# Kernel optimization log

Measured on AMD Instinct MI355X. Metric: run time of the kernel, lower is better.

Reference implementation:

```python
import jax, jax.numpy as jnp
import numpy as np

DIM = 1024
NUM_HEADS = 16
HEAD_DIM = DIM // NUM_HEADS


def setup_inputs() -> dict:
    key = jax.random.key(0)
    k1, k2, k3 = jax.random.split(key, 3)
    x = jax.random.normal(k1, (2, 2048, DIM), dtype=jnp.float32)
    # nn.Linear weights stored as [out, in]; apply as x @ W.T
    w_qkv = jax.random.normal(k2, (3 * DIM, DIM), dtype=jnp.float32) * (1.0 / np.sqrt(DIM))
    w_out = jax.random.normal(k3, (DIM, DIM), dtype=jnp.float32) * (1.0 / np.sqrt(DIM))
    return {"x": x, "w_qkv": w_qkv, "w_out": w_out}


def reference(x, w_qkv, w_out):
    b, t, _ = x.shape
    qkv = x @ w_qkv.T                                  # [b, t, 3*dim]
    qkv = qkv.reshape(b, t, 3, NUM_HEADS, HEAD_DIM)    # (three h d) split order
    q, k, v = jnp.moveaxis(qkv, 2, 0)                  # each [b, t, h, d]
    q = q.transpose(0, 2, 1, 3)                        # [b, h, t, d]
    k = k.transpose(0, 2, 1, 3)
    v = v.transpose(0, 2, 1, 3)
    attn = jnp.einsum('bhid,bhjd->bhij', q, k) / np.sqrt(HEAD_DIM)
    causal_mask = jnp.triu(jnp.ones((t, t), dtype=bool), k=1)
    attn = jnp.where(causal_mask, -jnp.inf, attn)
    attn = jax.nn.softmax(attn, axis=-1)
    out = jnp.einsum('bhij,bhjd->bhid', attn, v)
    out = out.transpose(0, 2, 1, 3).reshape(b, t, DIM)
    return out @ w_out.T
```

## Files before the change

### kernel.cpp

```cpp
#include <hip/hip_runtime.h>

#define DIM_ 1024
#define HEADS_ 16
#define HD_ 64
#define T_ 2048
#define BATCH_ 2
#define QKVN_ 3072

typedef unsigned short u16;
typedef unsigned int u32;
typedef float f32x4 __attribute__((ext_vector_type(4)));
typedef float f32x16 __attribute__((ext_vector_type(16)));
typedef short s16x8 __attribute__((ext_vector_type(8)));
typedef unsigned short u16x4 __attribute__((ext_vector_type(4)));

__device__ __forceinline__ u16 f2bf(float f) {
  unsigned u = __float_as_uint(f);
  u += 0x7fffu + ((u >> 16) & 1u);
  return (u16)(u >> 16);
}

__device__ __forceinline__ float fexp2(float x) {
  float r;
  asm("v_exp_f32 %0, %1" : "=v"(r) : "v"(x));
  return r;
}

__device__ __forceinline__ u32 cvtpk(float a, float b) {
  u32 r;
  asm("v_cvt_pk_bf16_f32 %0, %1, %2" : "=v"(r) : "v"(a), "v"(b));
  return r;
}

__global__ __launch_bounds__(256) void cvt_all(const float* __restrict__ x,
                                               const float* __restrict__ wqkv,
                                               const float* __restrict__ wout,
                                               u16* __restrict__ outbase) {
  int i = blockIdx.x * 256 + threadIdx.x;
  const float4* src;
  int off;
  if (i < 1048576) { src = (const float4*)x; off = i; }
  else if (i < 1835008) { src = (const float4*)wqkv; off = i - 1048576; }
  else { src = (const float4*)wout; off = i - 1835008; }
  float4 v = src[off];
  u16x4 o;
  o.x = f2bf(v.x); o.y = f2bf(v.y); o.z = f2bf(v.z); o.w = f2bf(v.w);
  reinterpret_cast<u16x4*>(outbase)[i] = o;
}

__device__ __forceinline__ void gld_lds16(const void* g, void* l) {
  auto gp = (__attribute__((address_space(1))) char*)(unsigned long long)g;
  auto lp = (__attribute__((address_space(3))) char*)(unsigned int)(unsigned long long)l;
  __builtin_amdgcn_global_load_lds(gp, lp, 16, 0, 0);
}

__global__ __launch_bounds__(256) void gemm_qkv(const u16* __restrict__ A,
                                                const u16* __restrict__ B,
                                                u16* __restrict__ qkvo,
                                                u16* __restrict__ vto,
                                                int M, int N, int K) {
  __shared__ __align__(16) u16 As[128 * 32];
  __shared__ __align__(16) u16 Bs[128 * 32];
  const int tid = threadIdx.x;
  const int lane = tid & 63;
  const int w = tid >> 6;
  const int wr = w >> 1, wc = w & 1;
  const int lrow = lane & 15, kg = lane >> 4;
  const int nt = blockIdx.x, mt = blockIdx.y;
  const u16* Ag = A + (size_t)(mt * 128) * K;
  const u16* Bg = B + (size_t)(nt * 128) * K;

  f32x4 acc[4][4];
#pragma unroll
  for (int i = 0; i < 4; ++i)
#pragma unroll
    for (int j = 0; j < 4; ++j) {
      f32x4 z = {0.f, 0.f, 0.f, 0.f};
      acc[i][j] = z;
    }

  const int e0 = tid * 8;
  const int row0 = e0 >> 5, kc0 = e0 & 31;
  const int row1 = row0 + 64, kc1 = kc0;
  const int ldsoff0 = (tid & ~63) * 16;
  const int ldsoff1 = (256 + (tid & ~63)) * 16;

  for (int k0 = 0; k0 < K; k0 += 32) {
    gld_lds16(Ag + (size_t)row0 * K + k0 + kc0, (char*)As + ldsoff0);
    gld_lds16(Ag + (size_t)row1 * K + k0 + kc1, (char*)As + ldsoff1);
    gld_lds16(Bg + (size_t)row0 * K + k0 + kc0, (char*)Bs + ldsoff0);
    gld_lds16(Bg + (size_t)row1 * K + k0 + kc1, (char*)Bs + ldsoff1);
    __syncthreads();
    s16x8 a[4], b[4];
#pragma unroll
    for (int mf = 0; mf < 4; ++mf)
      a[mf] = *(const s16x8*)&As[(wr * 64 + mf * 16 + lrow) * 32 + 8 * kg];
#pragma unroll
    for (int nf = 0; nf < 4; ++nf)
      b[nf] = *(const s16x8*)&Bs[(wc * 64 + nf * 16 + lrow) * 32 + 8 * kg];
#pragma unroll
    for (int mf = 0; mf < 4; ++mf)
#pragma unroll
      for (int nf = 0; nf < 4; ++nf)
        acc[mf][nf] = __builtin_amdgcn_mfma_f32_16x16x32_bf16(a[mf], b[nf], acc[mf][nf], 0, 0, 0);
    __syncthreads();
  }

  if (nt < 16) {
#pragma unroll
    for (int mf = 0; mf < 4; ++mf)
#pragma unroll
      for (int nf = 0; nf < 4; ++nf)
#pragma unroll
        for (int j = 0; j < 4; ++j) {
          int r = mt * 128 + wr * 64 + mf * 16 + 4 * kg + j;
          int c = nt * 128 + wc * 64 + nf * 16 + lrow;
          qkvo[(size_t)r * QKVN_ + c] = f2bf(acc[mf][nf][j]);
        }
  } else {
#pragma unroll
    for (int mf = 0; mf < 4; ++mf)
#pragma unroll
      for (int nf = 0; nf < 4; ++nf) {
        const int c = nt * 128 + wc * 64 + nf * 16 + lrow;
        const int d = c & 63, hV = (c >> 6) & 15;
        const int r0 = mt * 128 + wr * 64 + mf * 16 + 4 * kg;
        const int bb = r0 >> 11, t0 = r0 & 2047;
        u16x4 pk;
        pk.x = f2bf(acc[mf][nf][0]); pk.y = f2bf(acc[mf][nf][1]);
        pk.z = f2bf(acc[mf][nf][2]); pk.w = f2bf(acc[mf][nf][3]);
        *(u16x4*)(vto + ((size_t)(bb * 16 + hV) * 64 + d) * T_ + t0) = pk;
      }
  }
}

__global__ __launch_bounds__(256) void gemm_out(const u16* __restrict__ A,
                                                const u16* __restrict__ B,
                                                float* __restrict__ Cv,
                                                int M, int N, int K) {
  __shared__ __align__(16) u16 As[128 * 32];
  __shared__ __align__(16) u16 Bs[128 * 32];
  const int tid = threadIdx.x;
  const int lane = tid & 63;
  const int w = tid >> 6;
  const int wr = w >> 1, wc = w & 1;
  const int lrow = lane & 15, kg = lane >> 4;
  const int nt = blockIdx.x, mt = blockIdx.y;
  const u16* Ag = A + (size_t)(mt * 128) * K;
  const u16* Bg = B + (size_t)(nt * 128) * K;

  f32x4 acc[4][4];
#pragma unroll
  for (int i = 0; i < 4; ++i)
#pragma unroll
    for (int j = 0; j < 4; ++j) {
      f32x4 z = {0.f, 0.f, 0.f, 0.f};
      acc[i][j] = z;
    }

  const int e0 = tid * 8;
  const int row0 = e0 >> 5, kc0 = e0 & 31;
  const int row1 = row0 + 64, kc1 = kc0;
  const int ldsoff0 = (tid & ~63) * 16;
  const int ldsoff1 = (256 + (tid & ~63)) * 16;

  for (int k0 = 0; k0 < K; k0 += 32) {
    gld_lds16(Ag + (size_t)row0 * K + k0 + kc0, (char*)As + ldsoff0);
    gld_lds16(Ag + (size_t)row1 * K + k0 + kc1, (char*)As + ldsoff1);
    gld_lds16(Bg + (size_t)row0 * K + k0 + kc0, (char*)Bs + ldsoff0);
    gld_lds16(Bg + (size_t)row1 * K + k0 + kc1, (char*)Bs + ldsoff1);
    __syncthreads();
    s16x8 a[4], b[4];
#pragma unroll
    for (int mf = 0; mf < 4; ++mf)
      a[mf] = *(const s16x8*)&As[(wr * 64 + mf * 16 + lrow) * 32 + 8 * kg];
#pragma unroll
    for (int nf = 0; nf < 4; ++nf)
      b[nf] = *(const s16x8*)&Bs[(wc * 64 + nf * 16 + lrow) * 32 + 8 * kg];
#pragma unroll
    for (int mf = 0; mf < 4; ++mf)
#pragma unroll
      for (int nf = 0; nf < 4; ++nf)
        acc[mf][nf] = __builtin_amdgcn_mfma_f32_16x16x32_bf16(a[mf], b[nf], acc[mf][nf], 0, 0, 0);
    __syncthreads();
  }

#pragma unroll
  for (int mf = 0; mf < 4; ++mf)
#pragma unroll
    for (int nf = 0; nf < 4; ++nf)
#pragma unroll
      for (int j = 0; j < 4; ++j) {
        int r = mt * 128 + wr * 64 + mf * 16 + 4 * kg + j;
        int c = nt * 128 + wc * 64 + nf * 16 + lrow;
        Cv[(size_t)r * N + c] = acc[mf][nf][j];
      }
}

__global__ __launch_bounds__(256, 2) void attn_fwd(const u16* __restrict__ qkv,
                                                   const u16* __restrict__ vt,
                                                   u16* __restrict__ o) {
  const int gid = blockIdx.x;
  const int pr = gid >> 5;
  const int bh = gid & 31;
  const int b = bh >> 4, h = bh & 15;
  const int tid = threadIdx.x;
  const int lane = tid & 63;
  const int qw = (tid >> 6) & 1;
  const int kvg = tid >> 7;
  const int l31 = lane & 31, hi = lane >> 5;

  __shared__ __align__(16) char smem[65536];

  const int row_s = tid >> 3, slot_s = tid & 7;
  const u16* Kbase = qkv + (size_t)(b * T_) * QKVN_ + 1024 + h * 64;
  const u16* Vbase = vt + (size_t)(bh * 64) * T_;
  const u16* KgA = Kbase + (size_t)row_s * QKVN_ + slot_s * 8;
  const u16* KgB = KgA + (size_t)32 * QKVN_;
  const u16* VgA = Vbase + (size_t)row_s * T_ + slot_s * 8;
  const u16* VgB = VgA + (size_t)32 * T_;
  const int dstA = row_s * 128 + ((slot_s ^ (row_s & 7)) << 4);

  const int rbyte = l31 * 128;
  const int xsw = l31 & 7;
  const float CEXP = 0.18033688011112042f;

  for (int ph = 0; ph < 2; ++ph) {
    const int jt = (ph == 0) ? (31 - pr) : pr;
    const int nt = jt + 1;
    const int nrt = (nt + 1) >> 1;
    const int qrow0 = 64 * jt + 32 * qw;

    s16x8 qf[4];
    {
      const u16* qp = qkv + (size_t)(b * T_ + qrow0 + l31) * QKVN_ + h * 64 + 8 * hi;
#pragma unroll
      for (int ksl = 0; ksl < 4; ++ksl)
        qf[ksl] = *(const s16x8*)(qp + 16 * ksl);
    }

    f32x16 o0v, o1v;
#pragma unroll
    for (int r = 0; r < 16; ++r) { o0v[r] = 0.f; o1v[r] = 0.f; }
    float mrun = -__builtin_inff(), lrun = 0.0f;

    __syncthreads();
    *(s16x8*)(smem + dstA)                 = *(const s16x8*)KgA;
    *(s16x8*)(smem + 4096 + dstA)          = *(const s16x8*)KgB;
    *(s16x8*)(smem + 32768 + dstA)         = *(const s16x8*)VgA;
    *(s16x8*)(smem + 32768 + 4096 + dstA)  = *(const s16x8*)VgB;
    if (nt > 1) {
      *(s16x8*)(smem + 8192 + dstA)                = *(const s16x8*)(KgA + (size_t)64 * QKVN_);
      *(s16x8*)(smem + 8192 + 4096 + dstA)         = *(const s16x8*)(KgB + (size_t)64 * QKVN_);
      *(s16x8*)(smem + 32768 + 8192 + dstA)        = *(const s16x8*)(VgA + 64);
      *(s16x8*)(smem + 32768 + 8192 + 4096 + dstA) = *(const s16x8*)(VgB + 64);
    }

    int cur = 0;
    for (int r = 0; r < nrt; ++r) {
      const int t = 2 * r + kvg;
      const bool pe = (2 * r + 2 < nt), po = (2 * r + 3 < nt);
      s16x8 ke0, ke1, ve0, ve1, ko0, ko1, vo0, vo1;
      if (pe) {
        const size_t kofs = (size_t)(2 * r + 2) * 64 * QKVN_;
        const int vofs = (2 * r + 2) * 64;
        ke0 = *(const s16x8*)(KgA + kofs);
        ke1 = *(const s16x8*)(KgB + kofs);
        ve0 = *(const s16x8*)(VgA + vofs);
        ve1 = *(const s16x8*)(VgB + vofs);
      }
      if (po) {
        const size_t kofs = (size_t)(2 * r + 3) * 64 * QKVN_;
        const int vofs = (2 * r + 3) * 64;
        ko0 = *(const s16x8*)(KgA + kofs);
        ko1 = *(const s16x8*)(KgB + kofs);
        vo0 = *(const s16x8*)(VgA + vofs);
        vo1 = *(const s16x8*)(VgB + vofs);
      }
      __syncthreads();

      if (t < nt) {
        const char* Kc = smem + cur * 16384 + kvg * 8192;
        const char* Vc = smem + 32768 + cur * 16384 + kvg * 8192;
        const bool isdiag = (t == nt - 1);
        const bool two = !(isdiag && qw == 0);

        f32x16 s0v, s1v;
#pragma unroll
        for (int rr = 0; rr < 16; ++rr) { s0v[rr] = 0.f; s1v[rr] = 0.f; }
        __builtin_amdgcn_s_setprio(1);
#pragma unroll
        for (int ksl = 0; ksl < 4; ++ksl) {
          const s16x8 kf = *(const s16x8*)(Kc + rbyte + (((2 * ksl + hi) ^ xsw) << 4));
          s0v = __builtin_amdgcn_mfma_f32_32x32x16_bf16(kf, qf[ksl], s0v, 0, 0, 0);
        }
        if (two) {
#pragma unroll
          for (int ksl = 0; ksl < 4; ++ksl) {
            const s16x8 kf = *(const s16x8*)(Kc + 4096 + rbyte + (((2 * ksl + hi) ^ xsw) << 4));
            s1v = __builtin_amdgcn_mfma_f32_32x32x16_bf16(kf, qf[ksl], s1v, 0, 0, 0);
          }
        }
        __builtin_amdgcn_s_setprio(0);

        if (isdiag) {
          const int thr = 32 * qw + l31;
#pragma unroll
          for (int rr = 0; rr < 16; ++rr) {
            const int kvl = 4 * hi + (rr & 3) + 8 * (rr >> 2);
            if (kvl > thr) s0v[rr] = -__builtin_inff();
            if (two && kvl + 32 > thr) s1v[rr] = -__builtin_inff();
          }
        }

        float mloc = s0v[0];
#pragma unroll
        for (int rr = 1; rr < 16; ++rr) mloc = fmaxf(mloc, s0v[rr]);
        if (two) {
#pragma unroll
          for (int rr = 0; rr < 16; ++rr) mloc = fmaxf(mloc, s1v[rr]);
        }
        mloc = fmaxf(mloc, __shfl_xor(mloc, 32));

        const bool needfull = !((mloc - mrun) * CEXP <= 8.0f);
        if (__any(needfull)) {
          const float newm = fmaxf(mrun, mloc);
          const float sc = fexp2((mrun - newm) * CEXP);
          mrun = newm;
          lrun *= sc;
          o0v *= sc;
          o1v *= sc;
        }
        const float msc = mrun * CEXP;

        float rs = 0.0f;
        u32 pd0[8], pd1[8];
#pragma unroll
        for (int ri = 0; ri < 8; ++ri) {
          const float p0 = fexp2(__builtin_fmaf(s0v[2 * ri], CEXP, -msc));
          const float p1 = fexp2(__builtin_fmaf(s0v[2 * ri + 1], CEXP, -msc));
          rs += p0 + p1;
          pd0[ri] = cvtpk(p0, p1);
        }
        if (two) {
#pragma unroll
          for (int ri = 0; ri < 8; ++ri) {
            const float p0 = fexp2(__builtin_fmaf(s1v[2 * ri], CEXP, -msc));
            const float p1 = fexp2(__builtin_fmaf(s1v[2 * ri + 1], CEXP, -msc));
            rs += p0 + p1;
            pd1[ri] = cvtpk(p0, p1);
          }
        }
        rs += __shfl_xor(rs, 32);
        lrun += rs;

        __builtin_amdgcn_s_setprio(1);
#pragma unroll
        for (int kk = 0; kk < 4; ++kk) {
          if (kk >= 2 && !two) break;
          u32 x0, y0, x1, y1;
          if (kk == 0)      { x0 = pd0[0]; y0 = pd0[2]; x1 = pd0[1]; y1 = pd0[3]; }
          else if (kk == 1) { x0 = pd0[4]; y0 = pd0[6]; x1 = pd0[5]; y1 = pd0[7]; }
          else if (kk == 2) { x0 = pd1[0]; y0 = pd1[2]; x1 = pd1[1]; y1 = pd1[3]; }
          else              { x0 = pd1[4]; y0 = pd1[6]; x1 = pd1[5]; y1 = pd1[7]; }
          asm volatile("v_permlane32_swap_b32 %0, %1" : "+v"(x0), "+v"(y0));
          asm volatile("v_permlane32_swap_b32 %0, %1" : "+v"(x1), "+v"(y1));
          u32 pw[4] = {x0, x1, y0, y1};
          const s16x8 pf = *(const s16x8*)pw;
          const s16x8 vf0 = *(const s16x8*)(Vc + rbyte + (((2 * kk + hi) ^ xsw) << 4));
          const s16x8 vf1 = *(const s16x8*)(Vc + 4096 + rbyte + (((2 * kk + hi) ^ xsw) << 4));
          o0v = __builtin_amdgcn_mfma_f32_32x32x16_bf16(vf0, pf, o0v, 0, 0, 0);
          o1v = __builtin_amdgcn_mfma_f32_32x32x16_bf16(vf1, pf, o1v, 0, 0, 0);
        }
        __builtin_amdgcn_s_setprio(0);
      }

      if (pe) {
        const int nb = (cur ^ 1) * 16384;
        *(s16x8*)(smem + nb + dstA)                = ke0;
        *(s16x8*)(smem + nb + 4096 + dstA)         = ke1;
        *(s16x8*)(smem + 32768 + nb + dstA)        = ve0;
        *(s16x8*)(smem + 32768 + nb + 4096 + dstA) = ve1;
      }
      if (po) {
        const int nb = (cur ^ 1) * 16384 + 8192;
        *(s16x8*)(smem + nb + dstA)                = ko0;
        *(s16x8*)(smem + nb + 4096 + dstA)         = ko1;
        *(s16x8*)(smem + 32768 + nb + dstA)        = vo0;
        *(s16x8*)(smem + 32768 + nb + 4096 + dstA) = vo1;
      }
      cur ^= 1;
    }

    __syncthreads();
    float* Om = (float*)smem + qw * 2048;
    float* Mf = (float*)(smem + 16384) + qw * 64;
    float* Lf = (float*)(smem + 16896) + qw * 64;
    if (kvg == 1) {
#pragma unroll
      for (int rr = 0; rr < 16; ++rr) {
        Om[rr * 64 + lane] = o0v[rr];
        Om[(16 + rr) * 64 + lane] = o1v[rr];
      }
      Mf[lane] = mrun;
      Lf[lane] = lrun;
    }
    __syncthreads();
    if (kvg == 0) {
      const float mA = Mf[lane];
      const float lA = Lf[lane];
      const float m2 = fmaxf(mrun, mA);
      const float sB = fexp2((mrun - m2) * CEXP);
      const float sA = fexp2((mA - m2) * CEXP);
      const float linv = 1.0f / (lrun * sB + lA * sA);
      u16* orow = o + (size_t)(b * T_ + qrow0 + l31) * DIM_ + h * 64;
#pragma unroll
      for (int ri = 0; ri < 8; ++ri) {
        const int dbase0 = 4 * hi + 8 * (ri >> 1) + 2 * (ri & 1);
        const float a0 = (o0v[2 * ri] * sB + Om[(2 * ri) * 64 + lane] * sA) * linv;
        const float a1 = (o0v[2 * ri + 1] * sB + Om[(2 * ri + 1) * 64 + lane] * sA) * linv;
        const float c0 = (o1v[2 * ri] * sB + Om[(16 + 2 * ri) * 64 + lane] * sA) * linv;
        const float c1 = (o1v[2 * ri + 1] * sB + Om[(16 + 2 * ri + 1) * 64 + lane] * sA) * linv;
        *(u32*)(orow + dbase0) = cvtpk(a0, a1);
        *(u32*)(orow + 32 + dbase0) = cvtpk(c0, c1);
      }
    }
  }
}

extern "C" void kernel_launch(void* const* d_in, const int* in_sizes, int n_in,
                              void* d_out, int out_size, void* d_ws, size_t ws_size,
                              hipStream_t stream) {
  const float* x = (const float*)d_in[0];
  const float* w_qkv = (const float*)d_in[1];
  const float* w_out = (const float*)d_in[2];
  char* ws = (char*)d_ws;
  u16* xb    = (u16*)(ws + 0);
  u16* wqkvb = (u16*)(ws + 8388608);
  u16* woutb = (u16*)(ws + 14680064);
  u16* qkvb  = (u16*)(ws + 16777216);
  u16* vtb   = (u16*)(ws + 41943040);
  u16* attno = (u16*)(ws + 50331648);

  cvt_all<<<8192, 256, 0, stream>>>(x, w_qkv, w_out, xb);
  gemm_qkv<<<dim3(24, 32), 256, 0, stream>>>(xb, wqkvb, qkvb, vtb, 4096, 3072, 1024);
  attn_fwd<<<512, 256, 0, stream>>>(qkvb, vtb, attno);
  gemm_out<<<dim3(8, 32), 256, 0, stream>>>(attno, woutb, (float*)d_out, 4096, 1024, 1024);
}
```

Before: 112.4 us.

## Double-buffer GEMM LDS tiles, swizzle block order, and stage V-transpose through LDS

Merges the two GEMM kernels into one templated kernel that double-buffers the A/B LDS tiles, so global-to-LDS loads for the next K slice are issued before the MFMAs on the current slice and one barrier per iteration is dropped. Block IDs are remapped so that consecutive blocks share B tiles, which should improve L2 reuse. The transposed V epilogue now writes the tile to padded LDS and then emits 16-byte coalesced stores instead of scattered 8-byte writes. LDS use roughly doubles, which may reduce occupancy.

New measurement: 105.2 us. 1.07x faster.

```diff
diff --git a/kernel.cpp b/kernel.cpp
--- a/kernel.cpp
+++ b/kernel.cpp
@@ -54,19 +54,27 @@
   __builtin_amdgcn_global_load_lds(gp, lp, 16, 0, 0);
 }
 
-__global__ __launch_bounds__(256) void gemm_qkv(const u16* __restrict__ A,
-                                                const u16* __restrict__ B,
-                                                u16* __restrict__ qkvo,
-                                                u16* __restrict__ vto,
-                                                int M, int N, int K) {
-  __shared__ __align__(16) u16 As[128 * 32];
-  __shared__ __align__(16) u16 Bs[128 * 32];
+template <int MODE>
+__global__ __launch_bounds__(256) void gemm2(const u16* __restrict__ A,
+                                             const u16* __restrict__ B,
+                                             void* __restrict__ Cv,
+                                             u16* __restrict__ vto,
+                                             int N) {
+  __shared__ __align__(16) u16 smem[17408];
+  u16* As = smem;
+  u16* Bs = smem + 8192;
+  const int K = 1024;
+
+  const int bid = blockIdx.x;
+  const int cpx = gridDim.x >> 3;
+  const int swz = (bid & 7) * cpx + (bid >> 3);
+  const int nt = swz >> 5, mt = swz & 31;
+
   const int tid = threadIdx.x;
   const int lane = tid & 63;
   const int w = tid >> 6;
   const int wr = w >> 1, wc = w & 1;
   const int lrow = lane & 15, kg = lane >> 4;
-  const int nt = blockIdx.x, mt = blockIdx.y;
   const u16* Ag = A + (size_t)(mt * 128) * K;
   const u16* Bg = B + (size_t)(nt * 128) * K;
 
@@ -85,28 +93,52 @@
   const int ldsoff0 = (tid & ~63) * 16;
   const int ldsoff1 = (256 + (tid & ~63)) * 16;
 
+  gld_lds16(Ag + (size_t)row0 * K + kc0, (char*)As + ldsoff0);
+  gld_lds16(Ag + (size_t)row1 * K + kc1, (char*)As + ldsoff1);
+  gld_lds16(Bg + (size_t)row0 * K + kc0, (char*)Bs + ldsoff0);
+  gld_lds16(Bg + (size_t)row1 * K + kc1, (char*)Bs + ldsoff1);
+  __syncthreads();
+
+  int cur = 0;
   for (int k0 = 0; k0 < K; k0 += 32) {
-    gld_lds16(Ag + (size_t)row0 * K + k0 + kc0, (char*)As + ldsoff0);
-    gld_lds16(Ag + (size_t)row1 * K + k0 + kc1, (char*)As + ldsoff1);
-    gld_lds16(Bg + (size_t)row0 * K + k0 + kc0, (char*)Bs + ldsoff0);
-    gld_lds16(Bg + (size_t)row1 * K + k0 + kc1, (char*)Bs + ldsoff1);
-    __syncthreads();
+    if (k0 + 32 < K) {
+      const int nb = (cur ^ 1) * 8192;
+      gld_lds16(Ag + (size_t)row0 * K + k0 + 32 + kc0, (char*)As + nb + ldsoff0);
+      gld_lds16(Ag + (size_t)row1 * K + k0 + 32 + kc1, (char*)As + nb + ldsoff1);
+      gld_lds16(Bg + (size_t)row0 * K + k0 + 32 + kc0, (char*)Bs + nb + ldsoff0);
+      gld_lds16(Bg + (size_t)row1 * K + k0 + 32 + kc1, (char*)Bs + nb + ldsoff1);
+    }
+    const int cb = cur * 4096;
     s16x8 a[4], b[4];
 #pragma unroll
     for (int mf = 0; mf < 4; ++mf)
-      a[mf] = *(const s16x8*)&As[(wr * 64 + mf * 16 + lrow) * 32 + 8 * kg];
+      a[mf] = *(const s16x8*)&As[cb + (wr * 64 + mf * 16 + lrow) * 32 + 8 * kg];
 #pragma unroll
     for (int nf = 0; nf < 4; ++nf)
-      b[nf] = *(const s16x8*)&Bs[(wc * 64 + nf * 16 + lrow) * 32 + 8 * kg];
+      b[nf] = *(const s16x8*)&Bs[cb + (wc * 64 + nf * 16 + lrow) * 32 + 8 * kg];
 #pragma unroll
     for (int mf = 0; mf < 4; ++mf)
 #pragma unroll
       for (int nf = 0; nf < 4; ++nf)
         acc[mf][nf] = __builtin_amdgcn_mfma_f32_16x16x32_bf16(a[mf], b[nf], acc[mf][nf], 0, 0, 0);
     __syncthreads();
+    cur ^= 1;
   }
 
-  if (nt < 16) {
+  if (MODE == 1) {
+    float* C = (float*)Cv;
+#pragma unroll
+    for (int mf = 0; mf < 4; ++mf)
+#pragma unroll
+      for (int nf = 0; nf < 4; ++nf)
+#pragma unroll
+        for (int j = 0; j < 4; ++j) {
+          int r = mt * 128 + wr * 64 + mf * 16 + 4 * kg + j;
+          int c = nt * 128 + wc * 64 + nf * 16 + lrow;
+          C[(size_t)r * N + c] = acc[mf][nf][j];
+        }
+  } else if (nt < 16) {
+    u16* qkvo = (u16*)Cv;
 #pragma unroll
     for (int mf = 0; mf < 4; ++mf)
 #pragma unroll
@@ -118,83 +150,30 @@
           qkvo[(size_t)r * QKVN_ + c] = f2bf(acc[mf][nf][j]);
         }
   } else {
+    u16* Vlds = smem;
 #pragma unroll
     for (int mf = 0; mf < 4; ++mf)
 #pragma unroll
       for (int nf = 0; nf < 4; ++nf) {
-        const int c = nt * 128 + wc * 64 + nf * 16 + lrow;
-        const int d = c & 63, hV = (c >> 6) & 15;
-        const int r0 = mt * 128 + wr * 64 + mf * 16 + 4 * kg;
-        const int bb = r0 >> 11, t0 = r0 & 2047;
-        u16x4 pk;
-        pk.x = f2bf(acc[mf][nf][0]); pk.y = f2bf(acc[mf][nf][1]);
-        pk.z = f2bf(acc[mf][nf][2]); pk.w = f2bf(acc[mf][nf][3]);
-        *(u16x4*)(vto + ((size_t)(bb * 16 + hV) * 64 + d) * T_ + t0) = pk;
-      }
+        const int cl = wc * 64 + nf * 16 + lrow;
+        const int rl = wr * 64 + mf * 16 + 4 * kg;
+#pragma unroll
+        for (int j = 0; j < 4; ++j)
+          Vlds[cl * 136 + rl + j] = f2bf(acc[mf][nf][j]);
+      }
+    __syncthreads();
+    const int c16 = tid >> 4, chunk = tid & 15;
+    const int bb = mt >> 4;
+    const int tb = (mt & 15) * 128 + chunk * 8;
+#pragma unroll
+    for (int pass = 0; pass < 8; ++pass) {
+      const int cl = pass * 16 + c16;
+      const int cg = nt * 128 + cl;
+      const int hV = (cg >> 6) & 15, d = cg & 63;
+      const s16x8 v = *(const s16x8*)&Vlds[cl * 136 + chunk * 8];
+      *(s16x8*)(vto + ((size_t)((bb * 16 + hV) * 64 + d)) * T_ + tb) = v;
+    }
   }
-}
-
-__global__ __launch_bounds__(256) void gemm_out(const u16* __restrict__ A,
-                                                const u16* __restrict__ B,
-                                                float* __restrict__ Cv,
-                                                int M, int N, int K) {
-  __shared__ __align__(16) u16 As[128 * 32];
-  __shared__ __align__(16) u16 Bs[128 * 32];
-  const int tid = threadIdx.x;
-  const int lane = tid & 63;
-  const int w = tid >> 6;
-  const int wr = w >> 1, wc = w & 1;
-  const int lrow = lane & 15, kg = lane >> 4;
-  const int nt = blockIdx.x, mt = blockIdx.y;
-  const u16* Ag = A + (size_t)(mt * 128) * K;
-  const u16* Bg = B + (size_t)(nt * 128) * K;
-
-  f32x4 acc[4][4];
-#pragma unroll
-  for (int i = 0; i < 4; ++i)
-#pragma unroll
-    for (int j = 0; j < 4; ++j) {
-      f32x4 z = {0.f, 0.f, 0.f, 0.f};
-      acc[i][j] = z;
-    }
-
-  const int e0 = tid * 8;
-  const int row0 = e0 >> 5, kc0 = e0 & 31;
-  const int row1 = row0 + 64, kc1 = kc0;
-  const int ldsoff0 = (tid & ~63) * 16;
-  const int ldsoff1 = (256 + (tid & ~63)) * 16;
-
-  for (int k0 = 0; k0 < K; k0 += 32) {
-    gld_lds16(Ag + (size_t)row0 * K + k0 + kc0, (char*)As + ldsoff0);
-    gld_lds16(Ag + (size_t)row1 * K + k0 + kc1, (char*)As + ldsoff1);
-    gld_lds16(Bg + (size_t)row0 * K + k0 + kc0, (char*)Bs + ldsoff0);
-    gld_lds16(Bg + (size_t)row1 * K + k0 + kc1, (char*)Bs + ldsoff1);
-    __syncthreads();
-    s16x8 a[4], b[4];
-#pragma unroll
-    for (int mf = 0; mf < 4; ++mf)
-      a[mf] = *(const s16x8*)&As[(wr * 64 + mf * 16 + lrow) * 32 + 8 * kg];
-#pragma unroll
-    for (int nf = 0; nf < 4; ++nf)
-      b[nf] = *(const s16x8*)&Bs[(wc * 64 + nf * 16 + lrow) * 32 + 8 * kg];
-#pragma unroll
-    for (int mf = 0; mf < 4; ++mf)
-#pragma unroll
-      for (int nf = 0; nf < 4; ++nf)
-        acc[mf][nf] = __builtin_amdgcn_mfma_f32_16x16x32_bf16(a[mf], b[nf], acc[mf][nf], 0, 0, 0);
-    __syncthreads();
-  }
-
-#pragma unroll
-  for (int mf = 0; mf < 4; ++mf)
-#pragma unroll
-    for (int nf = 0; nf < 4; ++nf)
-#pragma unroll
-      for (int j = 0; j < 4; ++j) {
-        int r = mt * 128 + wr * 64 + mf * 16 + 4 * kg + j;
-        int c = nt * 128 + wc * 64 + nf * 16 + lrow;
-        Cv[(size_t)r * N + c] = acc[mf][nf][j];
-      }
 }
 
 __global__ __launch_bounds__(256, 2) void attn_fwd(const u16* __restrict__ qkv,
@@ -443,7 +422,7 @@
   u16* attno = (u16*)(ws + 50331648);
 
   cvt_all<<<8192, 256, 0, stream>>>(x, w_qkv, w_out, xb);
-  gemm_qkv<<<dim3(24, 32), 256, 0, stream>>>(xb, wqkvb, qkvb, vtb, 4096, 3072, 1024);
+  gemm2<2><<<768, 256, 0, stream>>>(xb, wqkvb, qkvb, vtb, QKVN_);
   attn_fwd<<<512, 256, 0, stream>>>(qkvb, vtb, attno);
-  gemm_out<<<dim3(8, 32), 256, 0, stream>>>(attno, woutb, (float*)d_out, 4096, 1024, 1024);
-}
+  gemm2<1><<<256, 256, 0, stream>>>(attno, woutb, d_out, nullptr, DIM_);
+}
```
